# Optimization experiments

Hardware: AMD Instinct MI355X
Metric: run time of the kernel (lower is better)

Reference implementation:

```python
import jax, jax.numpy as jnp
import numpy as np

IN_DIM = 256
QK_DIM = IN_DIM // 8


def setup_inputs() -> dict:
    key = jax.random.key(0)
    ks = jax.random.split(key, 7)
    B, C, H, W = 4, IN_DIM, 64, 64
    s = 0.05
    return {
        "x": jax.random.normal(ks[0], (B, C, H, W), dtype=jnp.float32),
        "Wq": jax.random.normal(ks[1], (QK_DIM, C), dtype=jnp.float32) * s,
        "bq": jnp.zeros((QK_DIM,), dtype=jnp.float32),
        "Wk": jax.random.normal(ks[2], (QK_DIM, C), dtype=jnp.float32) * s,
        "bk": jnp.zeros((QK_DIM,), dtype=jnp.float32),
        "Wv": jax.random.normal(ks[3], (C, C), dtype=jnp.float32) * s,
        "bv": jnp.zeros((C,), dtype=jnp.float32),
        "gamma": jnp.zeros((1,), dtype=jnp.float32),
    }


def reference(x, Wq, bq, Wk, bk, Wv, bv, gamma):
    B, C, H, W = x.shape
    N = H * W
    xf = x.reshape(B, C, N)  # [B, C, N]
    # 1x1 convs are channel matmuls
    q = jnp.einsum('oc,bcn->bno', Wq, xf) + bq  # [B, N, Cqk]
    k = jnp.einsum('oc,bcn->bon', Wk, xf) + bk[None, :, None]  # [B, Cqk, N]
    energy = jnp.einsum('bno,bom->bnm', q, k)  # [B, N, N]
    attn = jax.nn.softmax(energy, axis=-1)
    v = jnp.einsum('oc,bcn->bon', Wv, xf) + bv[None, :, None]  # [B, C, N]
    # torch: out = bmm(v, attn^T) -> out[b,c,m] = sum_n v[b,c,n]*attn[m,n]
    out = jnp.einsum('bcn,bmn->bcm', v, attn)
    out = out.reshape(B, C, H, W)
    return gamma[0] * out + x
```

## Files before the change

### kernel.cpp

```cpp
#include <hip/hip_runtime.h>
#include <hip/hip_bf16.h>
#include <cstddef>

#define NB  4
#define NC  256
#define NN  4096
#define DQK 32
#define MT  64
#define JT  64
#define NIT (NN / JT)
#define XS2 264

typedef __attribute__((ext_vector_type(8))) short short8;
typedef __attribute__((ext_vector_type(4))) float f32x4;

#define MFMA16(a, b, c) __builtin_amdgcn_mfma_f32_16x16x32_bf16((a), (b), (c), 0, 0, 0)

__device__ inline unsigned pk2bf(float a, float b) {
  __hip_bfloat162 h = __float22bfloat162_rn(make_float2(a, b));
  unsigned u;
  __builtin_memcpy(&u, &h, 4);
  return u;
}

__device__ inline void gl16(const void* g, void* s) {
  __builtin_amdgcn_global_load_lds(
      (const __attribute__((address_space(1))) void*)g,
      (__attribute__((address_space(3))) void*)s, 16, 0, 0);
}

__global__ __launch_bounds__(256) void wcvt_kernel(
    const float* __restrict__ Wq, const float* __restrict__ Wk,
    const float* __restrict__ Wv, __hip_bfloat16* __restrict__ W16) {
  const int id4 = (blockIdx.x * 256 + threadIdx.x) * 4;
  const int row = id4 >> 8, col = id4 & 255;
  const float* src = (row < 32) ? Wq + row * 256
                   : (row < 64) ? Wk + (row - 32) * 256
                                : Wv + (row - 64) * 256;
  float4 vv = *(const float4*)(src + col);
  *(uint2*)(W16 + id4) = make_uint2(pk2bf(vv.x, vv.y), pk2bf(vv.z, vv.w));
}

__global__ __launch_bounds__(256, 4) void proj_kernel(
    const float* __restrict__ x, const __hip_bfloat16* __restrict__ W16,
    const float* __restrict__ bq, const float* __restrict__ bk,
    const float* __restrict__ bv, __hip_bfloat16* __restrict__ q,
    __hip_bfloat16* __restrict__ kT, __hip_bfloat16* __restrict__ v) {
  __shared__ __hip_bfloat16 Xs[32 * XS2];
  const int t = threadIdx.x;
  const int b = blockIdx.y, n0 = blockIdx.x * 32;
  const int w = __builtin_amdgcn_readfirstlane(t >> 6);
  const int ln = t & 15, quad = (t & 63) >> 4;
  const int sn = t & 31, scg = t >> 5;

  const float* xsrc = x + (size_t)b * NC * NN + n0 + sn;
#pragma unroll
  for (int g = 0; g < 4; ++g) {
    float xr[8];
#pragma unroll
    for (int i = 0; i < 8; ++i)
      xr[i] = xsrc[(size_t)(g * 64 + scg * 8 + i) * NN];
    uint4 pw;
    pw.x = pk2bf(xr[0], xr[1]);
    pw.y = pk2bf(xr[2], xr[3]);
    pw.z = pk2bf(xr[4], xr[5]);
    pw.w = pk2bf(xr[6], xr[7]);
    *(uint4*)&Xs[sn * XS2 + g * 64 + scg * 8] = pw;
  }
  __syncthreads();

  f32x4 zero4 = {0.f, 0.f, 0.f, 0.f};
  f32x4 acc[5][2];
#pragma unroll
  for (int i = 0; i < 5; ++i)
#pragma unroll
    for (int j = 0; j < 2; ++j) acc[i][j] = zero4;

  const __hip_bfloat16* wbase = W16 + (size_t)(w * 80 + ln) * NC + quad * 8;
  short8 afc[5], afn[5];
#pragma unroll
  for (int ot = 0; ot < 5; ++ot)
    afc[ot] = *(const short8*)(wbase + (size_t)ot * 16 * NC);

#pragma unroll 1
  for (int k0 = 0; k0 < NC; k0 += 32) {
    const int kn = k0 + 32;
    if (kn < NC) {
#pragma unroll
      for (int ot = 0; ot < 5; ++ot)
        afn[ot] = *(const short8*)(wbase + (size_t)ot * 16 * NC + kn);
    }
    short8 bfr[2];
#pragma unroll
    for (int nt = 0; nt < 2; ++nt)
      bfr[nt] = *(const short8*)&Xs[(nt * 16 + ln) * XS2 + k0 + quad * 8];
#pragma unroll
    for (int ot = 0; ot < 5; ++ot)
#pragma unroll
      for (int nt = 0; nt < 2; ++nt)
        acc[ot][nt] = MFMA16(afc[ot], bfr[nt], acc[ot][nt]);
#pragma unroll
    for (int ot = 0; ot < 5; ++ot) afc[ot] = afn[ot];
  }

#pragma unroll
  for (int ot = 0; ot < 5; ++ot) {
    const int gbase = w * 80 + ot * 16;
    if (gbase < 32) {
#pragma unroll
      for (int nt = 0; nt < 2; ++nt)
#pragma unroll
        for (int r = 0; r < 4; ++r) {
          const int row = gbase + quad * 4 + r;
          q[((size_t)b * NN + n0 + nt * 16 + ln) * DQK + row] =
              __hip_bfloat16(acc[ot][nt][r] + bq[row]);
        }
    } else if (gbase < 64) {
#pragma unroll
      for (int nt = 0; nt < 2; ++nt)
#pragma unroll
        for (int r = 0; r < 4; ++r) {
          const int row = gbase - 32 + quad * 4 + r;
          kT[((size_t)b * NN + n0 + nt * 16 + ln) * DQK + row] =
              __hip_bfloat16(acc[ot][nt][r] + bk[row]);
        }
    } else {
#pragma unroll
      for (int nt = 0; nt < 2; ++nt)
#pragma unroll
        for (int r = 0; r < 4; ++r) {
          const int c = gbase - 64 + quad * 4 + r;
          v[((size_t)b * NC + c) * NN + n0 + nt * 16 + ln] =
              __hip_bfloat16(acc[ot][nt][r] + bv[c]);
        }
    }
  }
}

__global__ __launch_bounds__(512, 2) void flash_kernel(
    const __hip_bfloat16* __restrict__ q, const __hip_bfloat16* __restrict__ kt,
    const __hip_bfloat16* __restrict__ v, const float* __restrict__ x,
    const float* __restrict__ gamma, float* __restrict__ out) {
  __shared__ __align__(16) __hip_bfloat16 Ks[2][JT * DQK];
  __shared__ __align__(16) __hip_bfloat16 Vs[2][NC * JT];
  __shared__ __align__(16) __hip_bfloat16 Ps[2][MT * JT];
  __shared__ float lrow[MT];

  const int t  = threadIdx.x;
  const int bi = blockIdx.x;
  const int b  = (bi & 7) >> 1;
  const int m0 = (((bi & 1) * 32) + (bi >> 3)) * MT;

  const int w    = __builtin_amdgcn_readfirstlane(t >> 6);
  const int l    = t & 63;
  const int ln   = t & 15;
  const int quad = (t & 63) >> 4;

  const __hip_bfloat16* kb_base = kt + (size_t)b * NN * DQK;
  const __hip_bfloat16* v_base  = v + (size_t)b * NC * NN;

  size_t voff[4];
#pragma unroll
  for (int k = 0; k < 4; ++k) {
    const int g = w * 4 + k;
    const int c = g * 8 + (l >> 3);
    voff[k] = (size_t)c * NN + (((l & 7) ^ ((l >> 3) & 7)) * 8);
  }
  const size_t koff = (size_t)(w * 16 + (l >> 2)) * DQK +
                      (((l & 3) ^ ((l >> 2) & 3)) * 8);

  if (w < 4) gl16(kb_base + koff, &Ks[0][w * 512]);
  __syncthreads();

  if (w < 4) {
    const short8 qa =
        *(const short8*)(q + ((size_t)b * NN + m0 + w * 16 + ln) * DQK + quad * 8);
    float lreg = 0.f;
    const f32x4 zero4 = {0.f, 0.f, 0.f, 0.f};
    const int m = w * 16 + ln;

    for (int it = 0; it < NIT; ++it) {
#pragma unroll
      for (int k = 0; k < 4; ++k)
        gl16(v_base + voff[k] + (size_t)it * JT, &Vs[it & 1][(w * 4 + k) * 512]);
      if (it + 1 < NIT)
        gl16(kb_base + koff + (size_t)(it + 1) * JT * DQK, &Ks[(it + 1) & 1][w * 512]);

      short8 kb[4];
#pragma unroll
      for (int jt = 0; jt < 4; ++jt)
        kb[jt] = *(const short8*)&Ks[it & 1][(jt * 16 + ln) * DQK +
                                            ((quad ^ (ln & 3)) * 8)];
      f32x4 st[4];
      __builtin_amdgcn_s_setprio(1);
#pragma unroll
      for (int jt = 0; jt < 4; ++jt) st[jt] = MFMA16(kb[jt], qa, zero4);
      __builtin_amdgcn_s_setprio(0);

      char* pbase = (char*)&Ps[it & 1][0] + m * (JT * 2);
#pragma unroll
      for (int jt = 0; jt < 4; ++jt) {
        const float e0 = __expf(st[jt][0]), e1 = __expf(st[jt][1]);
        const float e2 = __expf(st[jt][2]), e3 = __expf(st[jt][3]);
        lreg += (e0 + e1) + (e2 + e3);
        *(uint2*)(pbase + ((jt * 32 + quad * 8) ^ ((m & 7) << 4))) =
            make_uint2(pk2bf(e0, e1), pk2bf(e2, e3));
      }
      __syncthreads();
    }
    lreg += __shfl_xor(lreg, 16);
    lreg += __shfl_xor(lreg, 32);
    if (quad == 0) lrow[w * 16 + ln] = lreg;
    __syncthreads();
  } else {
    const int c0 = (w - 4) * 64;
    const f32x4 zero4 = {0.f, 0.f, 0.f, 0.f};
    f32x4 acc[4][4];
#pragma unroll
    for (int ct = 0; ct < 4; ++ct)
#pragma unroll
      for (int mt = 0; mt < 4; ++mt) acc[ct][mt] = zero4;

    for (int it = 0; it < NIT; ++it) {
#pragma unroll
      for (int k = 0; k < 4; ++k)
        gl16(v_base + voff[k] + (size_t)it * JT, &Vs[it & 1][(w * 4 + k) * 512]);

      if (it > 0) {
        const int pbuf = (it - 1) & 1;
        const char* pbase = (const char*)&Ps[pbuf][0];
        short8 va[4][2];
#pragma unroll
        for (int ct = 0; ct < 4; ++ct)
#pragma unroll
          for (int ks = 0; ks < 2; ++ks)
            va[ct][ks] = *(const short8*)&Vs[pbuf][
                (c0 + ct * 16 + ln) * JT + (((ks * 4 + quad) ^ (ln & 7)) * 8)];
#pragma unroll
        for (int ks = 0; ks < 2; ++ks) {
          short8 pb[4];
#pragma unroll
          for (int mt = 0; mt < 4; ++mt)
            pb[mt] = *(const short8*)(pbase + (mt * 16 + ln) * (JT * 2) +
                                      ((ks * 64 + quad * 16) ^ ((ln & 7) << 4)));
          __builtin_amdgcn_s_setprio(1);
#pragma unroll
          for (int ct = 0; ct < 4; ++ct)
#pragma unroll
            for (int mt = 0; mt < 4; ++mt)
              acc[ct][mt] = MFMA16(va[ct][ks], pb[mt], acc[ct][mt]);
          __builtin_amdgcn_s_setprio(0);
        }
      }
      __syncthreads();
    }

    {
      const int pbuf = (NIT - 1) & 1;
      const char* pbase = (const char*)&Ps[pbuf][0];
      short8 va[4][2];
#pragma unroll
      for (int ct = 0; ct < 4; ++ct)
#pragma unroll
        for (int ks = 0; ks < 2; ++ks)
          va[ct][ks] = *(const short8*)&Vs[pbuf][
              (c0 + ct * 16 + ln) * JT + (((ks * 4 + quad) ^ (ln & 7)) * 8)];
#pragma unroll
      for (int ks = 0; ks < 2; ++ks) {
        short8 pb[4];
#pragma unroll
        for (int mt = 0; mt < 4; ++mt)
          pb[mt] = *(const short8*)(pbase + (mt * 16 + ln) * (JT * 2) +
                                    ((ks * 64 + quad * 16) ^ ((ln & 7) << 4)));
        __builtin_amdgcn_s_setprio(1);
#pragma unroll
        for (int ct = 0; ct < 4; ++ct)
#pragma unroll
          for (int mt = 0; mt < 4; ++mt)
            acc[ct][mt] = MFMA16(va[ct][ks], pb[mt], acc[ct][mt]);
        __builtin_amdgcn_s_setprio(0);
      }
    }
    __syncthreads();

    const float g0 = gamma[0];
    float li[4];
#pragma unroll
    for (int mt = 0; mt < 4; ++mt) li[mt] = 1.f / lrow[mt * 16 + ln];
#pragma unroll
    for (int ct = 0; ct < 4; ++ct)
#pragma unroll
      for (int r = 0; r < 4; ++r) {
        const int c = c0 + ct * 16 + quad * 4 + r;
        const float* xr = x + ((size_t)b * NC + c) * NN + m0;
        float* orow = out + ((size_t)b * NC + c) * NN + m0;
#pragma unroll
        for (int mt = 0; mt < 4; ++mt) {
          const int m = mt * 16 + ln;
          orow[m] = g0 * (acc[ct][mt][r] * li[mt]) + xr[m];
        }
      }
  }
}

extern "C" void kernel_launch(void* const* d_in, const int* in_sizes, int n_in,
                              void* d_out, int out_size, void* d_ws, size_t ws_size,
                              hipStream_t stream) {
  const float* x     = (const float*)d_in[0];
  const float* Wq    = (const float*)d_in[1];
  const float* bq    = (const float*)d_in[2];
  const float* Wk    = (const float*)d_in[3];
  const float* bk    = (const float*)d_in[4];
  const float* Wv    = (const float*)d_in[5];
  const float* bv    = (const float*)d_in[6];
  const float* gamma = (const float*)d_in[7];
  float* out = (float*)d_out;

  char* wsp = (char*)d_ws;
  __hip_bfloat16* W16 = (__hip_bfloat16*)wsp;  wsp += (size_t)320 * NC * 2;
  __hip_bfloat16* q   = (__hip_bfloat16*)wsp;  wsp += (size_t)NB * NN * DQK * 2;
  __hip_bfloat16* kT  = (__hip_bfloat16*)wsp;  wsp += (size_t)NB * NN * DQK * 2;
  __hip_bfloat16* v   = (__hip_bfloat16*)wsp;

  wcvt_kernel<<<dim3(80), dim3(256), 0, stream>>>(Wq, Wk, Wv, W16);
  proj_kernel<<<dim3(NN / 32, NB), dim3(256), 0, stream>>>(x, W16, bq, bk, bv, q, kT, v);
  flash_kernel<<<dim3(NB * NN / MT), dim3(512), 0, stream>>>(q, kT, v, x, gamma, out);
}
```

Before: 167.2 us.

## Fuse softmax and PV in-register across 16 waves, drop P LDS staging

Replaces the producer/consumer warp specialization (4 waves computing exp(QK) into LDS, 4 waves doing PV) with 16 uniform waves. Each wave recomputes QK^T for its 16-row m-tile and feeds the bf16 probabilities straight from registers into the PV MFMA for a 64-channel slice. This removes the P shared-memory round trip and the lrow exchange, and the V/K prefetch is now issued one iteration ahead. In exchange the QK and exp work is duplicated across four channel groups, the V operand is read with half-width LDS loads, and the block size grows to 1024 threads.

```diff
diff --git a/kernel.cpp b/kernel.cpp
--- a/kernel.cpp
+++ b/kernel.cpp
@@ -12,6 +12,7 @@
 #define XS2 264
 
 typedef __attribute__((ext_vector_type(8))) short short8;
+typedef __attribute__((ext_vector_type(4))) short short4v;
 typedef __attribute__((ext_vector_type(4))) float f32x4;
 
 #define MFMA16(a, b, c) __builtin_amdgcn_mfma_f32_16x16x32_bf16((a), (b), (c), 0, 0, 0)
@@ -137,14 +138,12 @@
   }
 }
 
-__global__ __launch_bounds__(512, 2) void flash_kernel(
+__global__ __launch_bounds__(1024, 4) void flash_kernel(
     const __hip_bfloat16* __restrict__ q, const __hip_bfloat16* __restrict__ kt,
     const __hip_bfloat16* __restrict__ v, const float* __restrict__ x,
     const float* __restrict__ gamma, float* __restrict__ out) {
   __shared__ __align__(16) __hip_bfloat16 Ks[2][JT * DQK];
   __shared__ __align__(16) __hip_bfloat16 Vs[2][NC * JT];
-  __shared__ __align__(16) __hip_bfloat16 Ps[2][MT * JT];
-  __shared__ float lrow[MT];
 
   const int t  = threadIdx.x;
   const int bi = blockIdx.x;
@@ -155,152 +154,110 @@
   const int l    = t & 63;
   const int ln   = t & 15;
   const int quad = (t & 63) >> 4;
+  const int mt_  = w & 3;
+  const int cq   = w >> 2;
 
   const __hip_bfloat16* kb_base = kt + (size_t)b * NN * DQK;
   const __hip_bfloat16* v_base  = v + (size_t)b * NC * NN;
 
-  size_t voff[4];
-#pragma unroll
-  for (int k = 0; k < 4; ++k) {
-    const int g = w * 4 + k;
-    const int c = g * 8 + (l >> 3);
-    voff[k] = (size_t)c * NN + (((l & 7) ^ ((l >> 3) & 7)) * 8);
+  size_t voff[2];
+#pragma unroll
+  for (int k = 0; k < 2; ++k) {
+    const int g = w * 2 + k;
+    voff[k] = (size_t)(g * 8 + (l >> 3)) * NN + (((l & 7) ^ ((l >> 3) & 7)) * 8);
   }
   const size_t koff = (size_t)(w * 16 + (l >> 2)) * DQK +
                       (((l & 3) ^ ((l >> 2) & 3)) * 8);
 
+#pragma unroll
+  for (int k = 0; k < 2; ++k)
+    gl16(v_base + voff[k], &Vs[0][(w * 2 + k) * 512]);
   if (w < 4) gl16(kb_base + koff, &Ks[0][w * 512]);
   __syncthreads();
 
-  if (w < 4) {
-    const short8 qa =
-        *(const short8*)(q + ((size_t)b * NN + m0 + w * 16 + ln) * DQK + quad * 8);
-    float lreg = 0.f;
-    const f32x4 zero4 = {0.f, 0.f, 0.f, 0.f};
-    const int m = w * 16 + ln;
-
-    for (int it = 0; it < NIT; ++it) {
-#pragma unroll
-      for (int k = 0; k < 4; ++k)
-        gl16(v_base + voff[k] + (size_t)it * JT, &Vs[it & 1][(w * 4 + k) * 512]);
-      if (it + 1 < NIT)
-        gl16(kb_base + koff + (size_t)(it + 1) * JT * DQK, &Ks[(it + 1) & 1][w * 512]);
-
-      short8 kb[4];
-#pragma unroll
-      for (int jt = 0; jt < 4; ++jt)
-        kb[jt] = *(const short8*)&Ks[it & 1][(jt * 16 + ln) * DQK +
-                                            ((quad ^ (ln & 3)) * 8)];
-      f32x4 st[4];
-      __builtin_amdgcn_s_setprio(1);
-#pragma unroll
-      for (int jt = 0; jt < 4; ++jt) st[jt] = MFMA16(kb[jt], qa, zero4);
-      __builtin_amdgcn_s_setprio(0);
-
-      char* pbase = (char*)&Ps[it & 1][0] + m * (JT * 2);
-#pragma unroll
-      for (int jt = 0; jt < 4; ++jt) {
-        const float e0 = __expf(st[jt][0]), e1 = __expf(st[jt][1]);
-        const float e2 = __expf(st[jt][2]), e3 = __expf(st[jt][3]);
-        lreg += (e0 + e1) + (e2 + e3);
-        *(uint2*)(pbase + ((jt * 32 + quad * 8) ^ ((m & 7) << 4))) =
-            make_uint2(pk2bf(e0, e1), pk2bf(e2, e3));
-      }
-      __syncthreads();
-    }
-    lreg += __shfl_xor(lreg, 16);
-    lreg += __shfl_xor(lreg, 32);
-    if (quad == 0) lrow[w * 16 + ln] = lreg;
-    __syncthreads();
-  } else {
-    const int c0 = (w - 4) * 64;
-    const f32x4 zero4 = {0.f, 0.f, 0.f, 0.f};
-    f32x4 acc[4][4];
-#pragma unroll
-    for (int ct = 0; ct < 4; ++ct)
-#pragma unroll
-      for (int mt = 0; mt < 4; ++mt) acc[ct][mt] = zero4;
-
-    for (int it = 0; it < NIT; ++it) {
-#pragma unroll
-      for (int k = 0; k < 4; ++k)
-        gl16(v_base + voff[k] + (size_t)it * JT, &Vs[it & 1][(w * 4 + k) * 512]);
-
-      if (it > 0) {
-        const int pbuf = (it - 1) & 1;
-        const char* pbase = (const char*)&Ps[pbuf][0];
-        short8 va[4][2];
-#pragma unroll
-        for (int ct = 0; ct < 4; ++ct)
-#pragma unroll
-          for (int ks = 0; ks < 2; ++ks)
-            va[ct][ks] = *(const short8*)&Vs[pbuf][
-                (c0 + ct * 16 + ln) * JT + (((ks * 4 + quad) ^ (ln & 7)) * 8)];
-#pragma unroll
-        for (int ks = 0; ks < 2; ++ks) {
-          short8 pb[4];
-#pragma unroll
-          for (int mt = 0; mt < 4; ++mt)
-            pb[mt] = *(const short8*)(pbase + (mt * 16 + ln) * (JT * 2) +
-                                      ((ks * 64 + quad * 16) ^ ((ln & 7) << 4)));
-          __builtin_amdgcn_s_setprio(1);
-#pragma unroll
-          for (int ct = 0; ct < 4; ++ct)
-#pragma unroll
-            for (int mt = 0; mt < 4; ++mt)
-              acc[ct][mt] = MFMA16(va[ct][ks], pb[mt], acc[ct][mt]);
-          __builtin_amdgcn_s_setprio(0);
-        }
-      }
-      __syncthreads();
-    }
-
-    {
-      const int pbuf = (NIT - 1) & 1;
-      const char* pbase = (const char*)&Ps[pbuf][0];
-      short8 va[4][2];
-#pragma unroll
-      for (int ct = 0; ct < 4; ++ct)
-#pragma unroll
-        for (int ks = 0; ks < 2; ++ks)
-          va[ct][ks] = *(const short8*)&Vs[pbuf][
-              (c0 + ct * 16 + ln) * JT + (((ks * 4 + quad) ^ (ln & 7)) * 8)];
+  const short8 qa =
+      *(const short8*)(q + ((size_t)b * NN + m0 + mt_ * 16 + ln) * DQK + quad * 8);
+  const f32x4 zero4 = {0.f, 0.f, 0.f, 0.f};
+  float lreg = 0.f;
+  f32x4 acc[4];
+#pragma unroll
+  for (int ct = 0; ct < 4; ++ct) acc[ct] = zero4;
+
+  for (int it = 0; it < NIT; ++it) {
+    const int buf = it & 1;
+    if (it + 1 < NIT) {
+#pragma unroll
+      for (int k = 0; k < 2; ++k)
+        gl16(v_base + voff[k] + (size_t)(it + 1) * JT, &Vs[buf ^ 1][(w * 2 + k) * 512]);
+      if (w < 4)
+        gl16(kb_base + koff + (size_t)(it + 1) * JT * DQK, &Ks[buf ^ 1][w * 512]);
+    }
+
+    short8 kb[4];
+#pragma unroll
+    for (int jt = 0; jt < 4; ++jt)
+      kb[jt] = *(const short8*)&Ks[buf][(jt * 16 + ln) * DQK + ((quad ^ (ln & 3)) * 8)];
+
+    f32x4 st[4];
+    __builtin_amdgcn_s_setprio(1);
+#pragma unroll
+    for (int jt = 0; jt < 4; ++jt) st[jt] = MFMA16(kb[jt], qa, zero4);
+    __builtin_amdgcn_s_setprio(0);
+
+    unsigned pkk[4][2];
+#pragma unroll
+    for (int jt = 0; jt < 4; ++jt) {
+      const float e0 = __expf(st[jt][0]), e1 = __expf(st[jt][1]);
+      const float e2 = __expf(st[jt][2]), e3 = __expf(st[jt][3]);
+      lreg += (e0 + e1) + (e2 + e3);
+      pkk[jt][0] = pk2bf(e0, e1);
+      pkk[jt][1] = pk2bf(e2, e3);
+    }
+    short8 pf[2];
+#pragma unroll
+    for (int ks = 0; ks < 2; ++ks) {
+      union { unsigned u[4]; short8 s; } cv;
+      cv.u[0] = pkk[2 * ks][0];
+      cv.u[1] = pkk[2 * ks][1];
+      cv.u[2] = pkk[2 * ks + 1][0];
+      cv.u[3] = pkk[2 * ks + 1][1];
+      pf[ks] = cv.s;
+    }
+
+    const char* vb = (const char*)&Vs[buf][0];
+#pragma unroll
+    for (int ct = 0; ct < 4; ++ct) {
+      const int c = cq * 64 + ct * 16 + ln;
+      const char* vr = vb + (size_t)c * 128;
 #pragma unroll
       for (int ks = 0; ks < 2; ++ks) {
-        short8 pb[4];
-#pragma unroll
-        for (int mt = 0; mt < 4; ++mt)
-          pb[mt] = *(const short8*)(pbase + (mt * 16 + ln) * (JT * 2) +
-                                    ((ks * 64 + quad * 16) ^ ((ln & 7) << 4)));
+        const int lcl = 4 * ks + (quad >> 1);
+        const int lch = lcl + 2;
+        const int half = (quad & 1) * 8;
+        union { short4v h[2]; short8 s; } vv;
+        vv.h[0] = *(const short4v*)(vr + ((lcl ^ (ln & 7)) * 16 + half));
+        vv.h[1] = *(const short4v*)(vr + ((lch ^ (ln & 7)) * 16 + half));
         __builtin_amdgcn_s_setprio(1);
-#pragma unroll
-        for (int ct = 0; ct < 4; ++ct)
-#pragma unroll
-          for (int mt = 0; mt < 4; ++mt)
-            acc[ct][mt] = MFMA16(va[ct][ks], pb[mt], acc[ct][mt]);
+        acc[ct] = MFMA16(vv.s, pf[ks], acc[ct]);
         __builtin_amdgcn_s_setprio(0);
       }
     }
     __syncthreads();
-
-    const float g0 = gamma[0];
-    float li[4];
-#pragma unroll
-    for (int mt = 0; mt < 4; ++mt) li[mt] = 1.f / lrow[mt * 16 + ln];
-#pragma unroll
-    for (int ct = 0; ct < 4; ++ct)
-#pragma unroll
-      for (int r = 0; r < 4; ++r) {
-        const int c = c0 + ct * 16 + quad * 4 + r;
-        const float* xr = x + ((size_t)b * NC + c) * NN + m0;
-        float* orow = out + ((size_t)b * NC + c) * NN + m0;
-#pragma unroll
-        for (int mt = 0; mt < 4; ++mt) {
-          const int m = mt * 16 + ln;
-          orow[m] = g0 * (acc[ct][mt][r] * li[mt]) + xr[m];
-        }
-      }
-  }
+  }
+
+  lreg += __shfl_xor(lreg, 16);
+  lreg += __shfl_xor(lreg, 32);
+  const float li = 1.f / lreg;
+
+  const float g0 = gamma[0];
+#pragma unroll
+  for (int ct = 0; ct < 4; ++ct)
+#pragma unroll
+    for (int r = 0; r < 4; ++r) {
+      const int c = cq * 64 + ct * 16 + quad * 4 + r;
+      const size_t base = ((size_t)b * NC + c) * NN + m0 + mt_ * 16;
+      out[base + ln] = g0 * (acc[ct][r] * li) + x[base + ln];
+    }
 }
 
 extern "C" void kernel_launch(void* const* d_in, const int* in_sizes, int n_in,
@@ -324,5 +281,5 @@
 
   wcvt_kernel<<<dim3(80), dim3(256), 0, stream>>>(Wq, Wk, Wv, W16);
   proj_kernel<<<dim3(NN / 32, NB), dim3(256), 0, stream>>>(x, W16, bq, bk, bv, q, kT, v);
-  flash_kernel<<<dim3(NB * NN / MT), dim3(512), 0, stream>>>(q, kT, v, x, gamma, out);
-}
+  flash_kernel<<<dim3(NB * NN / MT), dim3(1024), 0, stream>>>(q, kT, v, x, gamma, out);
+}
```

Measured after the change: 180.5 us. 1.08x slower.

## Triple-buffer V tiles, load K directly to registers, use explicit waitcnt barriers

Applied to the files above, without the earlier changes.

Drops the K shared-memory staging: producer warps load the next K tile straight into registers with a permuted row mapping, so the S tile comes out in a layout that can be stored to P as 16-byte swizzled writes. V moves to a three-stage shared buffer so loads for tile it+1 are issued while tile it-1 is consumed. The full __syncthreads is replaced by partial vmcnt waits plus s_barrier, so loads stay in flight across iterations. This adds shared memory (three V buffers) and relies on hand-counted vmcnt values, which is fragile if the load counts change.

```diff
diff --git a/kernel.cpp b/kernel.cpp
--- a/kernel.cpp
+++ b/kernel.cpp
@@ -141,8 +141,7 @@
     const __hip_bfloat16* __restrict__ q, const __hip_bfloat16* __restrict__ kt,
     const __hip_bfloat16* __restrict__ v, const float* __restrict__ x,
     const float* __restrict__ gamma, float* __restrict__ out) {
-  __shared__ __align__(16) __hip_bfloat16 Ks[2][JT * DQK];
-  __shared__ __align__(16) __hip_bfloat16 Vs[2][NC * JT];
+  __shared__ __align__(16) __hip_bfloat16 Vs[3][NC * JT];
   __shared__ __align__(16) __hip_bfloat16 Ps[2][MT * JT];
   __shared__ float lrow[MT];
 
@@ -161,56 +160,80 @@
 
   size_t voff[4];
 #pragma unroll
-  for (int k = 0; k < 4; ++k) {
-    const int g = w * 4 + k;
-    const int c = g * 8 + (l >> 3);
-    voff[k] = (size_t)c * NN + (((l & 7) ^ ((l >> 3) & 7)) * 8);
-  }
-  const size_t koff = (size_t)(w * 16 + (l >> 2)) * DQK +
-                      (((l & 3) ^ ((l >> 2) & 3)) * 8);
-
-  if (w < 4) gl16(kb_base + koff, &Ks[0][w * 512]);
-  __syncthreads();
+  for (int k = 0; k < 4; ++k)
+    voff[k] = (size_t)((w * 4 + k) * 8 + (l >> 3)) * NN +
+              (((l & 7) ^ ((l >> 3) & 7)) * 8);
+
+  const int swz0 = (((2 * quad + 0) ^ (ln & 7)) * 16);
+  const int swz1 = (((2 * quad + 1) ^ (ln & 7)) * 16);
+
+#pragma unroll
+  for (int k = 0; k < 4; ++k)
+    gl16(v_base + voff[k], &Vs[0][(w * 4 + k) * 512]);
 
   if (w < 4) {
     const short8 qa =
         *(const short8*)(q + ((size_t)b * NN + m0 + w * 16 + ln) * DQK + quad * 8);
+    const int rp = ((ln >> 2) & 3) * 16 + (ln & 3);
+    const f32x4 zero4 = {0.f, 0.f, 0.f, 0.f};
     float lreg = 0.f;
-    const f32x4 zero4 = {0.f, 0.f, 0.f, 0.f};
     const int m = w * 16 + ln;
-
-    for (int it = 0; it < NIT; ++it) {
-#pragma unroll
-      for (int k = 0; k < 4; ++k)
-        gl16(v_base + voff[k] + (size_t)it * JT, &Vs[it & 1][(w * 4 + k) * 512]);
-      if (it + 1 < NIT)
-        gl16(kb_base + koff + (size_t)(it + 1) * JT * DQK, &Ks[(it + 1) & 1][w * 512]);
-
-      short8 kb[4];
-#pragma unroll
-      for (int jt = 0; jt < 4; ++jt)
-        kb[jt] = *(const short8*)&Ks[it & 1][(jt * 16 + ln) * DQK +
-                                            ((quad ^ (ln & 3)) * 8)];
-      f32x4 st[4];
-      __builtin_amdgcn_s_setprio(1);
-#pragma unroll
-      for (int jt = 0; jt < 4; ++jt) st[jt] = MFMA16(kb[jt], qa, zero4);
-      __builtin_amdgcn_s_setprio(0);
-
-      char* pbase = (char*)&Ps[it & 1][0] + m * (JT * 2);
-#pragma unroll
-      for (int jt = 0; jt < 4; ++jt) {
-        const float e0 = __expf(st[jt][0]), e1 = __expf(st[jt][1]);
-        const float e2 = __expf(st[jt][2]), e3 = __expf(st[jt][3]);
-        lreg += (e0 + e1) + (e2 + e3);
-        *(uint2*)(pbase + ((jt * 32 + quad * 8) ^ ((m & 7) << 4))) =
-            make_uint2(pk2bf(e0, e1), pk2bf(e2, e3));
-      }
-      __syncthreads();
-    }
+    char* const prow0 = (char*)&Ps[0][0] + m * 128;
+    char* const prow1 = (char*)&Ps[1][0] + m * 128;
+    short8 kb0[4], kb1[4];
+#pragma unroll
+    for (int jt = 0; jt < 4; ++jt)
+      kb0[jt] = *(const short8*)(kb_base + (size_t)(rp + jt * 4) * DQK + quad * 8);
+    int sb = 1;
+
+#define PROD_STEP(IT, KBC, KBN, PROW)                                          \
+  do {                                                                         \
+    if ((IT) + 1 < NIT) {                                                      \
+      const size_t jn = (size_t)((IT) + 1) * JT;                               \
+      _Pragma("unroll") for (int k = 0; k < 4; ++k)                            \
+          gl16(v_base + voff[k] + jn, &Vs[sb][(w * 4 + k) * 512]);             \
+      _Pragma("unroll") for (int jt = 0; jt < 4; ++jt)                         \
+          KBN[jt] = *(const short8*)(kb_base + (jn + rp + jt * 4) * DQK +      \
+                                     quad * 8);                                \
+      asm volatile("s_waitcnt vmcnt(8)" ::: "memory");                         \
+    } else {                                                                   \
+      asm volatile("s_waitcnt vmcnt(0)" ::: "memory");                         \
+    }                                                                          \
+    f32x4 st[4];                                                               \
+    __builtin_amdgcn_s_setprio(1);                                             \
+    _Pragma("unroll") for (int jt = 0; jt < 4; ++jt)                           \
+        st[jt] = MFMA16(KBC[jt], qa, zero4);                                   \
+    __builtin_amdgcn_s_setprio(0);                                             \
+    unsigned pkk[4][2];                                                        \
+    _Pragma("unroll") for (int jt = 0; jt < 4; ++jt) {                         \
+      const float e0 = __expf(st[jt][0]), e1 = __expf(st[jt][1]);              \
+      const float e2 = __expf(st[jt][2]), e3 = __expf(st[jt][3]);              \
+      lreg += (e0 + e1) + (e2 + e3);                                           \
+      pkk[jt][0] = pk2bf(e0, e1);                                              \
+      pkk[jt][1] = pk2bf(e2, e3);                                              \
+    }                                                                          \
+    _Pragma("unroll") for (int ks = 0; ks < 2; ++ks) {                         \
+      union { unsigned u[4]; short8 s; } cv;                                   \
+      cv.u[0] = pkk[2 * ks][0];                                                \
+      cv.u[1] = pkk[2 * ks][1];                                                \
+      cv.u[2] = pkk[2 * ks + 1][0];                                            \
+      cv.u[3] = pkk[2 * ks + 1][1];                                            \
+      *(short8*)((PROW) + (ks ? swz1 : swz0)) = cv.s;                          \
+    }                                                                          \
+    sb = (sb == 2) ? 0 : sb + 1;                                               \
+    asm volatile("s_waitcnt lgkmcnt(0)" ::: "memory");                         \
+    __builtin_amdgcn_s_barrier();                                              \
+    asm volatile("" ::: "memory");                                             \
+  } while (0)
+
+    for (int it = 0; it < NIT; it += 2) {
+      PROD_STEP(it, kb0, kb1, prow0);
+      PROD_STEP(it + 1, kb1, kb0, prow1);
+    }
+#undef PROD_STEP
     lreg += __shfl_xor(lreg, 16);
     lreg += __shfl_xor(lreg, 32);
-    if (quad == 0) lrow[w * 16 + ln] = lreg;
+    if (quad == 0) lrow[m] = lreg;
     __syncthreads();
   } else {
     const int c0 = (w - 4) * 64;
@@ -221,28 +244,34 @@
 #pragma unroll
       for (int mt = 0; mt < 4; ++mt) acc[ct][mt] = zero4;
 
+    int sb = 1, rb = 2;
     for (int it = 0; it < NIT; ++it) {
-#pragma unroll
-      for (int k = 0; k < 4; ++k)
-        gl16(v_base + voff[k] + (size_t)it * JT, &Vs[it & 1][(w * 4 + k) * 512]);
-
+      if (it + 1 < NIT) {
+        const size_t jn = (size_t)(it + 1) * JT;
+#pragma unroll
+        for (int k = 0; k < 4; ++k)
+          gl16(v_base + voff[k] + jn, &Vs[sb][(w * 4 + k) * 512]);
+        asm volatile("s_waitcnt vmcnt(4)" ::: "memory");
+      } else {
+        asm volatile("s_waitcnt vmcnt(0)" ::: "memory");
+      }
       if (it > 0) {
-        const int pbuf = (it - 1) & 1;
-        const char* pbase = (const char*)&Ps[pbuf][0];
+        const char* vbb = (const char*)&Vs[rb][0];
+        const char* pbb = (const char*)&Ps[(it - 1) & 1][0];
         short8 va[4][2];
 #pragma unroll
-        for (int ct = 0; ct < 4; ++ct)
-#pragma unroll
-          for (int ks = 0; ks < 2; ++ks)
-            va[ct][ks] = *(const short8*)&Vs[pbuf][
-                (c0 + ct * 16 + ln) * JT + (((ks * 4 + quad) ^ (ln & 7)) * 8)];
+        for (int ct = 0; ct < 4; ++ct) {
+          const char* vr = vbb + (size_t)(c0 + ct * 16 + ln) * 128;
+          va[ct][0] = *(const short8*)(vr + swz0);
+          va[ct][1] = *(const short8*)(vr + swz1);
+        }
 #pragma unroll
         for (int ks = 0; ks < 2; ++ks) {
           short8 pb[4];
 #pragma unroll
           for (int mt = 0; mt < 4; ++mt)
-            pb[mt] = *(const short8*)(pbase + (mt * 16 + ln) * (JT * 2) +
-                                      ((ks * 64 + quad * 16) ^ ((ln & 7) << 4)));
+            pb[mt] = *(const short8*)(pbb + (size_t)(mt * 16 + ln) * 128 +
+                                      (ks ? swz1 : swz0));
           __builtin_amdgcn_s_setprio(1);
 #pragma unroll
           for (int ct = 0; ct < 4; ++ct)
@@ -252,26 +281,29 @@
           __builtin_amdgcn_s_setprio(0);
         }
       }
-      __syncthreads();
-    }
-
+      sb = (sb == 2) ? 0 : sb + 1;
+      rb = (rb == 2) ? 0 : rb + 1;
+      asm volatile("s_waitcnt lgkmcnt(0)" ::: "memory");
+      __builtin_amdgcn_s_barrier();
+      asm volatile("" ::: "memory");
+    }
     {
-      const int pbuf = (NIT - 1) & 1;
-      const char* pbase = (const char*)&Ps[pbuf][0];
+      const char* vbb = (const char*)&Vs[rb][0];
+      const char* pbb = (const char*)&Ps[(NIT - 1) & 1][0];
       short8 va[4][2];
 #pragma unroll
-      for (int ct = 0; ct < 4; ++ct)
-#pragma unroll
-        for (int ks = 0; ks < 2; ++ks)
-          va[ct][ks] = *(const short8*)&Vs[pbuf][
-              (c0 + ct * 16 + ln) * JT + (((ks * 4 + quad) ^ (ln & 7)) * 8)];
+      for (int ct = 0; ct < 4; ++ct) {
+        const char* vr = vbb + (size_t)(c0 + ct * 16 + ln) * 128;
+        va[ct][0] = *(const short8*)(vr + swz0);
+        va[ct][1] = *(const short8*)(vr + swz1);
+      }
 #pragma unroll
       for (int ks = 0; ks < 2; ++ks) {
         short8 pb[4];
 #pragma unroll
         for (int mt = 0; mt < 4; ++mt)
-          pb[mt] = *(const short8*)(pbase + (mt * 16 + ln) * (JT * 2) +
-                                    ((ks * 64 + quad * 16) ^ ((ln & 7) << 4)));
+          pb[mt] = *(const short8*)(pbb + (size_t)(mt * 16 + ln) * 128 +
+                                    (ks ? swz1 : swz0));
         __builtin_amdgcn_s_setprio(1);
 #pragma unroll
         for (int ct = 0; ct < 4; ++ct)
```

Result: slower. 178.4 us (+6.7%).

## Prefetch V/K two tiles ahead and replace syncthreads with vmcnt-counted barriers

Applied to the files above, without the earlier changes.

The V staging buffer grows from two to four stages and K from two to three, so loads for tile it+2 are issued while tile it is being consumed. The full __syncthreads is replaced by a barrier that waits only until the older global-to-LDS loads have landed (partial vmcnt), leaving the newest prefetch in flight. This aims to hide global load latency in the flash loop. In exchange it uses much more LDS (V grows from 64KB to 128KB), which may lower occupancy below the two-blocks-per-CU launch bound, and the vmcnt counts must match the exact number of outstanding loads per wave.

```diff
diff --git a/kernel.cpp b/kernel.cpp
--- a/kernel.cpp
+++ b/kernel.cpp
@@ -27,6 +27,14 @@
   __builtin_amdgcn_global_load_lds(
       (const __attribute__((address_space(1))) void*)g,
       (__attribute__((address_space(3))) void*)s, 16, 0, 0);
+}
+
+template <int N>
+__device__ inline void bar_vm() {
+  asm volatile("s_waitcnt lgkmcnt(0)" ::: "memory");
+  asm volatile("s_waitcnt vmcnt(%0)" ::"n"(N) : "memory");
+  __builtin_amdgcn_s_barrier();
+  asm volatile("" ::: "memory");
 }
 
 __global__ __launch_bounds__(256) void wcvt_kernel(
@@ -141,8 +149,8 @@
     const __hip_bfloat16* __restrict__ q, const __hip_bfloat16* __restrict__ kt,
     const __hip_bfloat16* __restrict__ v, const float* __restrict__ x,
     const float* __restrict__ gamma, float* __restrict__ out) {
-  __shared__ __align__(16) __hip_bfloat16 Ks[2][JT * DQK];
-  __shared__ __align__(16) __hip_bfloat16 Vs[2][NC * JT];
+  __shared__ __align__(16) __hip_bfloat16 Vs[4][NC * JT];
+  __shared__ __align__(16) __hip_bfloat16 Ks[3][JT * DQK];
   __shared__ __align__(16) __hip_bfloat16 Ps[2][MT * JT];
   __shared__ float lrow[MT];
 
@@ -161,18 +169,23 @@
 
   size_t voff[4];
 #pragma unroll
-  for (int k = 0; k < 4; ++k) {
-    const int g = w * 4 + k;
-    const int c = g * 8 + (l >> 3);
-    voff[k] = (size_t)c * NN + (((l & 7) ^ ((l >> 3) & 7)) * 8);
-  }
+  for (int k = 0; k < 4; ++k)
+    voff[k] = (size_t)((w * 4 + k) * 8 + (l >> 3)) * NN +
+              (((l & 7) ^ ((l >> 3) & 7)) * 8);
   const size_t koff = (size_t)(w * 16 + (l >> 2)) * DQK +
                       (((l & 3) ^ ((l >> 2) & 3)) * 8);
 
-  if (w < 4) gl16(kb_base + koff, &Ks[0][w * 512]);
-  __syncthreads();
+#pragma unroll
+  for (int j = 0; j < 2; ++j) {
+#pragma unroll
+    for (int k = 0; k < 4; ++k)
+      gl16(v_base + voff[k] + (size_t)j * JT, &Vs[j][(w * 4 + k) * 512]);
+    if (w < 4)
+      gl16(kb_base + koff + (size_t)j * JT * DQK, &Ks[j][w * 512]);
+  }
 
   if (w < 4) {
+    bar_vm<5>();
     const short8 qa =
         *(const short8*)(q + ((size_t)b * NN + m0 + w * 16 + ln) * DQK + quad * 8);
     float lreg = 0.f;
@@ -180,17 +193,20 @@
     const int m = w * 16 + ln;
 
     for (int it = 0; it < NIT; ++it) {
-#pragma unroll
-      for (int k = 0; k < 4; ++k)
-        gl16(v_base + voff[k] + (size_t)it * JT, &Vs[it & 1][(w * 4 + k) * 512]);
-      if (it + 1 < NIT)
-        gl16(kb_base + koff + (size_t)(it + 1) * JT * DQK, &Ks[(it + 1) & 1][w * 512]);
+      const bool more = (it + 2 < NIT);
+      if (more) {
+        const size_t jn = (size_t)(it + 2) * JT;
+#pragma unroll
+        for (int k = 0; k < 4; ++k)
+          gl16(v_base + voff[k] + jn, &Vs[(it + 2) & 3][(w * 4 + k) * 512]);
+        gl16(kb_base + koff + jn * DQK, &Ks[(it + 2) % 3][w * 512]);
+      }
 
       short8 kb[4];
 #pragma unroll
       for (int jt = 0; jt < 4; ++jt)
-        kb[jt] = *(const short8*)&Ks[it & 1][(jt * 16 + ln) * DQK +
-                                            ((quad ^ (ln & 3)) * 8)];
+        kb[jt] = *(const short8*)&Ks[it % 3][(jt * 16 + ln) * DQK +
+                                             ((quad ^ (ln & 3)) * 8)];
       f32x4 st[4];
       __builtin_amdgcn_s_setprio(1);
 #pragma unroll
@@ -206,13 +222,14 @@
         *(uint2*)(pbase + ((jt * 32 + quad * 8) ^ ((m & 7) << 4))) =
             make_uint2(pk2bf(e0, e1), pk2bf(e2, e3));
       }
-      __syncthreads();
+      if (more) bar_vm<5>(); else bar_vm<0>();
     }
     lreg += __shfl_xor(lreg, 16);
     lreg += __shfl_xor(lreg, 32);
-    if (quad == 0) lrow[w * 16 + ln] = lreg;
+    if (quad == 0) lrow[m] = lreg;
     __syncthreads();
   } else {
+    bar_vm<8>();
     const int c0 = (w - 4) * 64;
     const f32x4 zero4 = {0.f, 0.f, 0.f, 0.f};
     f32x4 acc[4][4];
@@ -222,26 +239,30 @@
       for (int mt = 0; mt < 4; ++mt) acc[ct][mt] = zero4;
 
     for (int it = 0; it < NIT; ++it) {
-#pragma unroll
-      for (int k = 0; k < 4; ++k)
-        gl16(v_base + voff[k] + (size_t)it * JT, &Vs[it & 1][(w * 4 + k) * 512]);
-
+      const bool more = (it + 2 < NIT);
+      if (more) {
+        const size_t jn = (size_t)(it + 2) * JT;
+#pragma unroll
+        for (int k = 0; k < 4; ++k)
+          gl16(v_base + voff[k] + jn, &Vs[(it + 2) & 3][(w * 4 + k) * 512]);
+      }
       if (it > 0) {
-        const int pbuf = (it - 1) & 1;
-        const char* pbase = (const char*)&Ps[pbuf][0];
+        const char* vbb = (const char*)&Vs[(it - 1) & 3][0];
+        const char* pbb = (const char*)&Ps[(it - 1) & 1][0];
         short8 va[4][2];
 #pragma unroll
         for (int ct = 0; ct < 4; ++ct)
 #pragma unroll
           for (int ks = 0; ks < 2; ++ks)
-            va[ct][ks] = *(const short8*)&Vs[pbuf][
-                (c0 + ct * 16 + ln) * JT + (((ks * 4 + quad) ^ (ln & 7)) * 8)];
+            va[ct][ks] = *(const short8*)(vbb +
+                (size_t)(c0 + ct * 16 + ln) * (JT * 2) +
+                (((ks * 4 + quad) ^ (ln & 7)) * 16));
 #pragma unroll
         for (int ks = 0; ks < 2; ++ks) {
           short8 pb[4];
 #pragma unroll
           for (int mt = 0; mt < 4; ++mt)
-            pb[mt] = *(const short8*)(pbase + (mt * 16 + ln) * (JT * 2) +
+            pb[mt] = *(const short8*)(pbb + (size_t)(mt * 16 + ln) * (JT * 2) +
                                       ((ks * 64 + quad * 16) ^ ((ln & 7) << 4)));
           __builtin_amdgcn_s_setprio(1);
 #pragma unroll
@@ -252,25 +273,26 @@
           __builtin_amdgcn_s_setprio(0);
         }
       }
-      __syncthreads();
+      if (more) bar_vm<8>(); else bar_vm<0>();
     }
 
     {
-      const int pbuf = (NIT - 1) & 1;
-      const char* pbase = (const char*)&Ps[pbuf][0];
+      const char* vbb = (const char*)&Vs[(NIT - 1) & 3][0];
+      const char* pbb = (const char*)&Ps[(NIT - 1) & 1][0];
       short8 va[4][2];
 #pragma unroll
       for (int ct = 0; ct < 4; ++ct)
 #pragma unroll
         for (int ks = 0; ks < 2; ++ks)
-          va[ct][ks] = *(const short8*)&Vs[pbuf][
-              (c0 + ct * 16 + ln) * JT + (((ks * 4 + quad) ^ (ln & 7)) * 8)];
+          va[ct][ks] = *(const short8*)(vbb +
+              (size_t)(c0 + ct * 16 + ln) * (JT * 2) +
+              (((ks * 4 + quad) ^ (ln & 7)) * 16));
 #pragma unroll
       for (int ks = 0; ks < 2; ++ks) {
         short8 pb[4];
 #pragma unroll
         for (int mt = 0; mt < 4; ++mt)
-          pb[mt] = *(const short8*)(pbase + (mt * 16 + ln) * (JT * 2) +
+          pb[mt] = *(const short8*)(pbb + (size_t)(mt * 16 + ln) * (JT * 2) +
                                     ((ks * 64 + quad * 16) ^ ((ln & 7) << 4)));
         __builtin_amdgcn_s_setprio(1);
 #pragma unroll
```

After: 162.7 us. 2.7% less time.
